# Performance work log

Hardware: AMD Instinct MI355X
Metric: run time of the kernel (lower is better)

The kernel has to match this reference:

```python
import jax, jax.numpy as jnp
from jax import lax
import numpy as np

P = 4        # pool_size
NH = 8       # nhead
EPS = 1e-5


def _maxpool(x):
    return lax.reduce_window(x, -jnp.inf, lax.max, (1, 1, P, P), (1, 1, P, P), 'VALID')


def _ln_c(x, g, b):
    # LayerNorm over channel dim of NCHW (torch applies it on NHWC last dim)
    m = x.mean(1, keepdims=True)
    v = x.var(1, keepdims=True)
    return g[None, :, None, None] * (x - m) / jnp.sqrt(v + EPS) + b[None, :, None, None]


def _dwbn(x, w, g, b, rm, rv):
    # depthwise 3x3 conv (groups=C, no bias) + BatchNorm2d (inference, running stats)
    C = x.shape[1]
    y = lax.conv_general_dilated(x, w, (1, 1), ((1, 1), (1, 1)),
                                 dimension_numbers=('NCHW', 'OIHW', 'NCHW'),
                                 feature_group_count=C)
    sc = g / jnp.sqrt(rv + EPS)
    return sc[None, :, None, None] * (y - rm[None, :, None, None]) + b[None, :, None, None]


def _heads(x):
    # n (nhead d) h w -> n (h w) nhead d
    B, C, H, W = x.shape
    return x.reshape(B, NH, C // NH, H * W).transpose(0, 3, 1, 2)


def _fuse(x, m, merge_w, mlp_w1, mlp_w2, ln2_g, ln2_b):
    # merge linear -> reshape to pooled map -> bilinear upsample x4 -> concat -> MLP -> LN -> residual
    B, C, H, W = x.shape
    m = jnp.einsum('nlh d -> nlhd', m) if False else m  # no-op, keep m as [B,L,NH,dim]
    m = m.reshape(B, -1, C) @ merge_w.T                  # [B, L, C]
    m = m.reshape(B, H // P, W // P, C).transpose(0, 3, 1, 2)
    m = jax.image.resize(m, (B, C, H, W), method='bilinear')  # align_corners=False convention
    z = jnp.concatenate([x, m], axis=1).transpose(0, 2, 3, 1)  # NHWC, 2C
    z = jax.nn.relu(z @ mlp_w1.T) @ mlp_w2.T                   # [B,H,W,C]
    mu = z.mean(-1, keepdims=True)
    var = z.var(-1, keepdims=True)
    z = ln2_g * (z - mu) / jnp.sqrt(var + EPS) + ln2_b
    return x + z.transpose(0, 3, 1, 2)


def setup_inputs() -> dict:
    key = jax.random.key(0)
    ks = jax.random.split(key, 20)
    B, C, H, W = 4, 256, 128, 128
    s = 0.05
    return {
        'x1': jax.random.normal(ks[0], (B, C, H, W), jnp.float32),
        'x2': jax.random.normal(ks[1], (B, C, H, W), jnp.float32),
        'qk_w': jax.random.normal(ks[2], (C, 1, 3, 3), jnp.float32) * s,
        'qk_g': 1.0 + 0.1 * jax.random.normal(ks[3], (C,), jnp.float32),
        'qk_b': 0.1 * jax.random.normal(ks[4], (C,), jnp.float32),
        'qk_m': 0.1 * jax.random.normal(ks[5], (C,), jnp.float32),
        'qk_v': jax.random.uniform(ks[6], (C,), jnp.float32, 0.5, 1.5),
        'v_w': jax.random.normal(ks[7], (C, 1, 3, 3), jnp.float32) * s,
        'v_g': 1.0 + 0.1 * jax.random.normal(ks[8], (C,), jnp.float32),
        'v_b': 0.1 * jax.random.normal(ks[9], (C,), jnp.float32),
        'v_m': 0.1 * jax.random.normal(ks[10], (C,), jnp.float32),
        'v_v': jax.random.uniform(ks[11], (C,), jnp.float32, 0.5, 1.5),
        'ln1_g': 1.0 + 0.1 * jax.random.normal(ks[12], (C,), jnp.float32),
        'ln1_b': 0.1 * jax.random.normal(ks[13], (C,), jnp.float32),
        'ln2_g': 1.0 + 0.1 * jax.random.normal(ks[14], (C,), jnp.float32),
        'ln2_b': 0.1 * jax.random.normal(ks[15], (C,), jnp.float32),
        'merge_w': jax.random.normal(ks[16], (C, C), jnp.float32) * s,
        'mlp_w1': jax.random.normal(ks[17], (2 * C, 2 * C), jnp.float32) * s,
        'mlp_w2': jax.random.normal(ks[18], (C, 2 * C), jnp.float32) * s,
    }


def reference(x1, x2, qk_w, qk_g, qk_b, qk_m, qk_v, v_w, v_g, v_b, v_m, v_v,
              ln1_g, ln1_b, ln2_g, ln2_b, merge_w, mlp_w1, mlp_w2):
    # pooled + normalized features (norm1 shared across q/k/v branches)
    p1 = _ln_c(_maxpool(x1), ln1_g, ln1_b)
    p2 = _ln_c(_maxpool(x2), ln1_g, ln1_b)
    query = _heads(_dwbn(p1, qk_w, qk_g, qk_b, qk_m, qk_v))  # [B,L,NH,d]
    key = _heads(_dwbn(p2, qk_w, qk_g, qk_b, qk_m, qk_v))    # [B,S,NH,d]
    v1h = _heads(_dwbn(p1, v_w, v_g, v_b, v_m, v_v))
    v2h = _heads(_dwbn(p2, v_w, v_g, v_b, v_m, v_v))
    QK = jnp.einsum('nlhd,nshd->nlsh', query, key).astype(jnp.float32)
    t = 1.0 / np.sqrt(query.shape[-1]).astype(np.float32)
    S1 = jax.nn.softmax(t * QK, axis=2)   # softmax over s (keys)
    S2 = jax.nn.softmax(t * QK, axis=3)   # softmax over head dim (as in source)
    m1 = jnp.einsum('nlsh,nshd->nlhd', S1, v2h)
    m2 = jnp.einsum('nlsh,nlhd->nshd', S2, v1h)
    out1 = _fuse(x1, m1, merge_w, mlp_w1, mlp_w2, ln2_g, ln2_b)
    out2 = _fuse(x2, m2, merge_w, mlp_w1, mlp_w2, ln2_g, ln2_b)
    return (out1, out2)
```

## Files before the change

### kernel.cpp

```cpp
#include <hip/hip_runtime.h>
#include <hip/hip_bf16.h>

#define NB 4
#define NC 256
#define NH_ 8
#define LPOOL 1024
constexpr float EPSV = 1e-5f;

typedef unsigned short ushort_t;
typedef __attribute__((ext_vector_type(8))) short bf16x8;
typedef __attribute__((ext_vector_type(4))) float f32x4;

#define OFF_P   0u
#define OFF_V2T 1048576u
#define OFF_Q   2097152u
#define OFF_K   3145728u
#define OFF_V1  4194304u
#define OFF_V2  5242880u
#define OFF_M1  6291456u
#define OFF_M2  7340032u
#define OFF_MG  8388608u
#define OFF_A   9437184u
#define OFF_W1B 26214400u
#define OFF_W2B 26345472u
#define OFF_WCB 26411008u

__device__ __forceinline__ float bf16_to_f(unsigned short u) {
    union { unsigned int ui; float f; } t; t.ui = ((unsigned int)u) << 16; return t.f;
}
__device__ __forceinline__ unsigned short f_to_bf16(float f) {
    union { float f; unsigned int u; } t; t.f = f;
    unsigned int u = t.u;
    u += 0x7fffu + ((u >> 16) & 1u);
    return (unsigned short)(u >> 16);
}

__global__ __launch_bounds__(256) void pool_kernel(const float* __restrict__ x1,
                                                   const float* __restrict__ x2,
                                                   float* __restrict__ pooled) {
    int idx = blockIdx.x * 256 + threadIdx.x;
    int j = idx & 31, i = (idx >> 5) & 31, c = (idx >> 10) & 255, n = (idx >> 18) & 3, br = idx >> 20;
    const float* xp = br ? x2 : x1;
    const float* base = xp + (((size_t)(n * 256 + c) * 128 + i * 4) * 128 + j * 4);
    float m = -3.4e38f;
#pragma unroll
    for (int r = 0; r < 4; ++r) {
        float4 v = *(const float4*)(base + r * 128);
        m = fmaxf(m, fmaxf(fmaxf(v.x, v.y), fmaxf(v.z, v.w)));
    }
    pooled[(size_t)br * 1048576 + (size_t)(n * 256 + c) * 1024 + i * 32 + j] = m;
}

__global__ __launch_bounds__(256) void lnc_kernel(float* __restrict__ p,
                                                  const float* __restrict__ g,
                                                  const float* __restrict__ b) {
    int bid = blockIdx.x;
    int l = bid & 1023, n = (bid >> 10) & 3, br = bid >> 12;
    int c = threadIdx.x;
    size_t idx = (size_t)br * 1048576 + (size_t)(n * 256 + c) * 1024 + l;
    float v = p[idx];
    __shared__ float red[256];
    red[c] = v; __syncthreads();
    for (int off = 128; off > 0; off >>= 1) { if (c < off) red[c] += red[c + off]; __syncthreads(); }
    float mean = red[0] / 256.f;
    __syncthreads();
    float d = v - mean;
    red[c] = d * d; __syncthreads();
    for (int off = 128; off > 0; off >>= 1) { if (c < off) red[c] += red[c + off]; __syncthreads(); }
    float var = red[0] / 256.f;
    float rstd = rsqrtf(var + EPSV);
    p[idx] = (v - mean) * rstd * g[c] + b[c];
}

__global__ __launch_bounds__(256) void dwbn_kernel(const float* __restrict__ p,
    const float* __restrict__ qkw, const float* __restrict__ qkg, const float* __restrict__ qkb,
    const float* __restrict__ qkm, const float* __restrict__ qkv,
    const float* __restrict__ vw, const float* __restrict__ vg, const float* __restrict__ vb,
    const float* __restrict__ vm, const float* __restrict__ vv,
    float* __restrict__ qkvbuf) {
    int which = blockIdx.y;
    int flat = blockIdx.x * 256 + threadIdx.x;
    int l = flat & 1023, c = (flat >> 10) & 255, n = flat >> 18;
    int br = which & 1;
    const float* w  = (which < 2) ? qkw : vw;
    const float* g  = (which < 2) ? qkg : vg;
    const float* bb = (which < 2) ? qkb : vb;
    const float* rm = (which < 2) ? qkm : vm;
    const float* rv = (which < 2) ? qkv : vv;
    int i = l >> 5, j = l & 31;
    const float* pin = p + (size_t)br * 1048576 + (size_t)(n * 256 + c) * 1024;
    float acc = 0.f;
#pragma unroll
    for (int ky = -1; ky <= 1; ++ky) {
        int yy = i + ky;
        if ((unsigned)yy < 32u) {
#pragma unroll
            for (int kx = -1; kx <= 1; ++kx) {
                int xx = j + kx;
                if ((unsigned)xx < 32u)
                    acc += pin[yy * 32 + xx] * w[c * 9 + (ky + 1) * 3 + (kx + 1)];
            }
        }
    }
    float sc = g[c] * rsqrtf(rv[c] + EPSV);
    qkvbuf[(size_t)which * 1048576 + (size_t)(n * 1024 + l) * 256 + c] = sc * (acc - rm[c]) + bb[c];
}

__global__ __launch_bounds__(256) void cvt_kernel(const float* __restrict__ in,
                                                  ushort_t* __restrict__ out, int n) {
    int i = blockIdx.x * 256 + threadIdx.x;
    if (i < n) out[i] = f_to_bf16(in[i]);
}

__global__ __launch_bounds__(256) void wc_kernel(const float* __restrict__ w1,
                                                 const float* __restrict__ mw,
                                                 ushort_t* __restrict__ wcb) {
    int r = blockIdx.x, t = threadIdx.x;
    __shared__ float wrow[256];
    wrow[t] = w1[(size_t)r * 512 + 256 + t];
    __syncthreads();
    float acc = 0.f;
    for (int c = 0; c < 256; ++c) acc += wrow[c] * mw[(size_t)c * 256 + t];
    wcb[(size_t)r * 256 + t] = f_to_bf16(acc);
}

__global__ __launch_bounds__(256) void v2t_kernel(const float* __restrict__ v,
                                                  ushort_t* __restrict__ vt) {
    int bid = blockIdx.x;
    int sb = bid & 31, cb = (bid >> 5) & 7, n = bid >> 8;
    int tid = threadIdx.x;
    __shared__ float t[32][33];
    int ci = tid & 31, sg = tid >> 5;
#pragma unroll
    for (int p = 0; p < 4; ++p) {
        int s = sb * 32 + p * 8 + sg;
        t[p * 8 + sg][ci] = v[(size_t)(n * 1024 + s) * 256 + cb * 32 + ci];
    }
    __syncthreads();
    int si = tid & 31, cg = tid >> 5;
#pragma unroll
    for (int p = 0; p < 4; ++p) {
        int c = cb * 32 + p * 8 + cg;
        vt[(size_t)(n * 256 + c) * 1024 + sb * 32 + si] = f_to_bf16(t[si][p * 8 + cg]);
    }
}

__global__ __launch_bounds__(256) void qk_mfma(const ushort_t* __restrict__ qb,
                                               const ushort_t* __restrict__ kb,
                                               ushort_t* __restrict__ scores) {
    int lt = blockIdx.x, st = blockIdx.y;
    int nh = blockIdx.z; int n = nh >> 3, h = nh & 7;
    int l0 = lt * 128, s0 = st * 128;
    __shared__ ushort_t Qs[128 * 32];
    __shared__ ushort_t Ks[128 * 32];
    int tid = threadIdx.x, lane = tid & 63, wv = tid >> 6;
    int wm = wv >> 1, wn = wv & 1;
    int ml = lane & 15, quad = lane >> 4;
#pragma unroll
    for (int c = 0; c < 2; ++c) {
        int g = c * 256 + tid;
        int row = g >> 2, seg = g & 3;
        const ushort_t* ga = qb + (size_t)(n * 1024 + l0 + row) * 256 + h * 32 + seg * 8;
        __builtin_amdgcn_global_load_lds((const __attribute__((address_space(1))) void*)ga,
                                         (__attribute__((address_space(3))) void*)&Qs[row * 32 + seg * 8], 16, 0, 0);
        const ushort_t* gk = kb + (size_t)(n * 1024 + s0 + row) * 256 + h * 32 + seg * 8;
        __builtin_amdgcn_global_load_lds((const __attribute__((address_space(1))) void*)gk,
                                         (__attribute__((address_space(3))) void*)&Ks[row * 32 + seg * 8], 16, 0, 0);
    }
    __syncthreads();
    f32x4 acc[4][4];
#pragma unroll
    for (int i = 0; i < 4; ++i)
#pragma unroll
        for (int j = 0; j < 4; ++j) acc[i][j] = (f32x4)(0.f);
    bf16x8 af[4], bfr[4];
#pragma unroll
    for (int mt = 0; mt < 4; ++mt)
        af[mt] = *(const bf16x8*)&Qs[(wm * 64 + mt * 16 + ml) * 32 + quad * 8];
#pragma unroll
    for (int nt = 0; nt < 4; ++nt)
        bfr[nt] = *(const bf16x8*)&Ks[(wn * 64 + nt * 16 + ml) * 32 + quad * 8];
#pragma unroll
    for (int mt = 0; mt < 4; ++mt)
#pragma unroll
        for (int nt = 0; nt < 4; ++nt)
            acc[mt][nt] = __builtin_amdgcn_mfma_f32_16x16x32_bf16(af[mt], bfr[nt], acc[mt][nt], 0, 0, 0);
    const float tsc = 0.17677669529663687f;
    ushort_t* sb = scores + (size_t)nh * 1024 * 1024;
#pragma unroll
    for (int mt = 0; mt < 4; ++mt)
#pragma unroll
        for (int nt = 0; nt < 4; ++nt) {
            int col = s0 + wn * 64 + nt * 16 + ml;
#pragma unroll
            for (int r = 0; r < 4; ++r) {
                int row = l0 + wm * 64 + mt * 16 + quad * 4 + r;
                unsigned short b = f_to_bf16(tsc * acc[mt][nt][r]);
                int partner = __shfl_xor((int)b, 1);
                if (!(ml & 1)) {
                    unsigned int pk = (unsigned int)b | ((unsigned int)partner << 16);
                    *(unsigned int*)&sb[(size_t)row * 1024 + col] = pk;
                }
            }
        }
}

__global__ __launch_bounds__(256) void m1_kernel(const ushort_t* __restrict__ scores,
                                                 const ushort_t* __restrict__ v2t,
                                                 ushort_t* __restrict__ m1out) {
    int lt = blockIdx.x, h = blockIdx.y, n = blockIdx.z;
    int tid = threadIdx.x, lane = tid & 63, wv = tid >> 6;
    int ml = lane & 15, quad = lane >> 4;
    int l0 = lt * 64 + wv * 16;
    const ushort_t* arow = scores + (size_t)((n * 8 + h) * 1024 + l0 + ml) * 1024 + quad * 8;
    const ushort_t* vb = v2t + (size_t)(n * 256 + h * 32) * 1024;
    const ushort_t* vrow0 = vb + (size_t)ml * 1024 + quad * 8;
    const ushort_t* vrow1 = vb + (size_t)(ml + 16) * 1024 + quad * 8;
    f32x4 acc0 = (f32x4)(0.f), acc1 = (f32x4)(0.f);
    float rsum = 0.f;
#pragma unroll 4
    for (int s0 = 0; s0 < 1024; s0 += 32) {
        bf16x8 sv = *(const bf16x8*)(arow + s0);
        float e0 = __expf(bf16_to_f((ushort_t)sv[0]));
        float e1 = __expf(bf16_to_f((ushort_t)sv[1]));
        float e2 = __expf(bf16_to_f((ushort_t)sv[2]));
        float e3 = __expf(bf16_to_f((ushort_t)sv[3]));
        float e4 = __expf(bf16_to_f((ushort_t)sv[4]));
        float e5 = __expf(bf16_to_f((ushort_t)sv[5]));
        float e6 = __expf(bf16_to_f((ushort_t)sv[6]));
        float e7 = __expf(bf16_to_f((ushort_t)sv[7]));
        rsum += ((e0 + e1) + (e2 + e3)) + ((e4 + e5) + (e6 + e7));
        bf16x8 af;
        af[0] = (short)f_to_bf16(e0); af[1] = (short)f_to_bf16(e1);
        af[2] = (short)f_to_bf16(e2); af[3] = (short)f_to_bf16(e3);
        af[4] = (short)f_to_bf16(e4); af[5] = (short)f_to_bf16(e5);
        af[6] = (short)f_to_bf16(e6); af[7] = (short)f_to_bf16(e7);
        bf16x8 b0 = *(const bf16x8*)(vrow0 + s0);
        bf16x8 b1 = *(const bf16x8*)(vrow1 + s0);
        acc0 = __builtin_amdgcn_mfma_f32_16x16x32_bf16(af, b0, acc0, 0, 0, 0);
        acc1 = __builtin_amdgcn_mfma_f32_16x16x32_bf16(af, b1, acc1, 0, 0, 0);
    }
    rsum += __shfl_xor(rsum, 16);
    rsum += __shfl_xor(rsum, 32);
#pragma unroll
    for (int r = 0; r < 4; ++r) {
        int row = quad * 4 + r;
        float inv = 1.f / __shfl(rsum, row);
        size_t ob = (size_t)(n * 1024 + l0 + row) * 256 + h * 32;
        m1out[ob + ml] = f_to_bf16(acc0[r] * inv);
        m1out[ob + 16 + ml] = f_to_bf16(acc1[r] * inv);
    }
}

__global__ __launch_bounds__(256) void m2_kernel(const ushort_t* __restrict__ scores,
                                                 const float* __restrict__ v1,
                                                 float* __restrict__ m2out) {
    int st = blockIdx.x;
    int lc = blockIdx.y;
    int n  = blockIdx.z;
    int s0 = st * 32, tid = threadIdx.x;
    __shared__ float wls[8][8][32];
    float acc[32];
#pragma unroll
    for (int i = 0; i < 32; ++i) acc[i] = 0.f;
    int lA = tid >> 5, siA = tid & 31;
    int hB = tid >> 5;
    const ushort_t* sbase = scores + (size_t)n * 8 * 1024 * 1024;
    int lend = lc * 128 + 128;
    for (int lb = lc * 128; lb < lend; lb += 8) {
        int l = lb + lA;
        float e[8];
        float mx = -3.4e38f;
#pragma unroll
        for (int h = 0; h < 8; ++h) {
            e[h] = bf16_to_f(sbase[((size_t)h * 1024 + l) * 1024 + s0 + siA]);
            mx = fmaxf(mx, e[h]);
        }
        float sum = 0.f;
#pragma unroll
        for (int h = 0; h < 8; ++h) { e[h] = expf(e[h] - mx); sum += e[h]; }
        float inv = 1.f / sum;
#pragma unroll
        for (int h = 0; h < 8; ++h) wls[lA][h][siA] = e[h] * inv;
        __syncthreads();
#pragma unroll
        for (int ls = 0; ls < 8; ++ls) {
            float v1v = v1[(size_t)(n * 1024 + lb + ls) * 256 + tid];
#pragma unroll
            for (int s4 = 0; s4 < 8; ++s4) {
                float4 w4 = *(const float4*)&wls[ls][hB][s4 * 4];
                acc[s4 * 4]     += w4.x * v1v;
                acc[s4 * 4 + 1] += w4.y * v1v;
                acc[s4 * 4 + 2] += w4.z * v1v;
                acc[s4 * 4 + 3] += w4.w * v1v;
            }
        }
        __syncthreads();
    }
#pragma unroll
    for (int ss = 0; ss < 32; ++ss)
        atomicAdd(&m2out[(size_t)(n * 1024 + s0 + ss) * 256 + tid], acc[ss]);
}

__global__ __launch_bounds__(256) void mfma_gemm(const ushort_t* __restrict__ A,
                                                 const ushort_t* __restrict__ B,
                                                 float* __restrict__ Of,
                                                 ushort_t* __restrict__ Oh,
                                                 int N, int relu, int K) {
    int m0 = blockIdx.x * 128, n0 = blockIdx.y * 128;
    int tid = threadIdx.x;
    __shared__ ushort_t Al[128 * 32];
    __shared__ ushort_t Bl[128 * 32];
    int lane = tid & 63;
    int wv = tid >> 6;
    int wm = wv >> 1, wn = wv & 1;
    int ml = lane & 15, quad = lane >> 4;
    f32x4 acc[4][4];
#pragma unroll
    for (int i = 0; i < 4; ++i)
#pragma unroll
        for (int j = 0; j < 4; ++j) acc[i][j] = (f32x4)(0.f);

    for (int k0 = 0; k0 < K; k0 += 32) {
#pragma unroll
        for (int c = 0; c < 2; ++c) {
            int g = c * 256 + tid;
            int row = g >> 2, seg = g & 3;
            const ushort_t* ga = A + (size_t)(m0 + row) * K + k0 + seg * 8;
            __builtin_amdgcn_global_load_lds((const __attribute__((address_space(1))) void*)ga,
                                             (__attribute__((address_space(3))) void*)&Al[g * 8], 16, 0, 0);
            const ushort_t* gb = B + (size_t)(n0 + row) * K + k0 + seg * 8;
            __builtin_amdgcn_global_load_lds((const __attribute__((address_space(1))) void*)gb,
                                             (__attribute__((address_space(3))) void*)&Bl[g * 8], 16, 0, 0);
        }
        __syncthreads();
        bf16x8 af[4], bfr[4];
#pragma unroll
        for (int mt = 0; mt < 4; ++mt)
            af[mt] = *(const bf16x8*)&Al[(wm * 64 + mt * 16 + ml) * 32 + quad * 8];
#pragma unroll
        for (int nt = 0; nt < 4; ++nt)
            bfr[nt] = *(const bf16x8*)&Bl[(wn * 64 + nt * 16 + ml) * 32 + quad * 8];
#pragma unroll
        for (int mt = 0; mt < 4; ++mt)
#pragma unroll
            for (int nt = 0; nt < 4; ++nt)
                acc[mt][nt] = __builtin_amdgcn_mfma_f32_16x16x32_bf16(af[mt], bfr[nt], acc[mt][nt], 0, 0, 0);
        __syncthreads();
    }
#pragma unroll
    for (int mt = 0; mt < 4; ++mt) {
#pragma unroll
        for (int nt = 0; nt < 4; ++nt) {
            int col = n0 + wn * 64 + nt * 16 + ml;
#pragma unroll
            for (int r = 0; r < 4; ++r) {
                int row = m0 + wm * 64 + mt * 16 + quad * 4 + r;
                float v = acc[mt][nt][r];
                if (relu) v = fmaxf(v, 0.f);
                if (Oh) Oh[(size_t)row * N + col] = f_to_bf16(v);
                else    Of[(size_t)row * N + col] = v;
            }
        }
    }
}

__global__ __launch_bounds__(256) void gemm1_fused(const float* __restrict__ x,
                                                   const ushort_t* __restrict__ W1,
                                                   const ushort_t* __restrict__ mm1,
                                                   ushort_t* __restrict__ hid) {
    __shared__ char smem[49152];
    ushort_t* Abf = (ushort_t*)smem;
    ushort_t* Bl  = (ushort_t*)(smem + 32768);
    float* t32    = (float*)(smem + 32768);
    int m0 = blockIdx.x * 64;
    int n = m0 >> 14, y = (m0 >> 7) & 127, x0 = m0 & 127;
    int n0 = blockIdx.y * 256;
    int tid = threadIdx.x, lane = tid & 63;
    int wv = tid >> 6, ml = lane & 15, quad = lane >> 4;

    const float* xrow = x + ((size_t)(n * 256) * 128 + y) * 128 + x0;
    for (int cb = 0; cb < 256; cb += 32) {
        __syncthreads();
        {
            int l16 = tid & 15, cl = tid >> 4;
#pragma unroll
            for (int pp = 0; pp < 2; ++pp) {
                int c = cb + pp * 16 + cl;
                float4 v = *(const float4*)(xrow + (size_t)c * 16384 + l16 * 4);
                *(float4*)&t32[(pp * 16 + cl) * 68 + l16 * 4] = v;
            }
        }
        __syncthreads();
        {
            int clw = tid & 31, pg = tid >> 5;
#pragma unroll
            for (int k = 0; k < 8; ++k) {
                int pix = pg * 8 + k;
                float v = t32[clw * 68 + pix];
                unsigned byte = ((unsigned)(pix * 256 + cb + clw) * 2u) ^ ((unsigned)(pix & 7) << 4);
                *(ushort_t*)(smem + byte) = f_to_bf16(v);
            }
        }
    }
    __syncthreads();

    f32x4 acc[4][4];
#pragma unroll
    for (int i = 0; i < 4; ++i)
#pragma unroll
        for (int j = 0; j < 4; ++j) acc[i][j] = (f32x4)(0.f);
    for (int k0 = 0; k0 < 256; k0 += 32) {
#pragma unroll
        for (int c = 0; c < 4; ++c) {
            int g = c * 256 + tid;
            int row = g >> 2, seg = g & 3;
            const ushort_t* gb = W1 + (size_t)(n0 + row) * 512 + k0 + seg * 8;
            __builtin_amdgcn_global_load_lds((const __attribute__((address_space(1))) void*)gb,
                                             (__attribute__((address_space(3))) void*)&Bl[g * 8], 16, 0, 0);
        }
        __syncthreads();
        bf16x8 af[4], bfr[4];
#pragma unroll
        for (int mt = 0; mt < 4; ++mt) {
            int pix = mt * 16 + ml;
            unsigned byte = ((unsigned)(pix * 256 + k0 + quad * 8) * 2u) ^ ((unsigned)(pix & 7) << 4);
            af[mt] = *(const bf16x8*)(smem + byte);
        }
#pragma unroll
        for (int nt = 0; nt < 4; ++nt)
            bfr[nt] = *(const bf16x8*)&Bl[(wv * 64 + nt * 16 + ml) * 32 + quad * 8];
#pragma unroll
        for (int mt = 0; mt < 4; ++mt)
#pragma unroll
            for (int nt = 0; nt < 4; ++nt)
                acc[mt][nt] = __builtin_amdgcn_mfma_f32_16x16x32_bf16(af[mt], bfr[nt], acc[mt][nt], 0, 0, 0);
        __syncthreads();
    }

    float iy = y * 0.25f - 0.375f;
    int y0i = (int)floorf(iy);
    float fy = iy - (float)y0i;
    int y0c = max(y0i, 0), y1c = min(y0i + 1, 31);
    const ushort_t* mb0 = mm1 + (size_t)(n * 1024 + y0c * 32) * 512;
    const ushort_t* mb1 = mm1 + (size_t)(n * 1024 + y1c * 32) * 512;
#pragma unroll
    for (int mt = 0; mt < 4; ++mt)
#pragma unroll
        for (int r = 0; r < 4; ++r) {
            int p = mt * 16 + quad * 4 + r;
            int xx = x0 + p;
            float ix = xx * 0.25f - 0.375f;
            int x0i = (int)floorf(ix);
            float fx = ix - (float)x0i;
            int xc0 = max(x0i, 0), xc1 = min(x0i + 1, 31);
#pragma unroll
            for (int nt = 0; nt < 4; ++nt) {
                int col = n0 + wv * 64 + nt * 16 + ml;
                float v00 = bf16_to_f(mb0[(size_t)xc0 * 512 + col]);
                float v01 = bf16_to_f(mb0[(size_t)xc1 * 512 + col]);
                float v10 = bf16_to_f(mb1[(size_t)xc0 * 512 + col]);
                float v11 = bf16_to_f(mb1[(size_t)xc1 * 512 + col]);
                float up = (1.f - fy) * ((1.f - fx) * v00 + fx * v01)
                         + fy * ((1.f - fx) * v10 + fx * v11);
                float v = fmaxf(acc[mt][nt][r] + up, 0.f);
                hid[(size_t)(m0 + p) * 512 + col] = f_to_bf16(v);
            }
        }
}

__global__ __launch_bounds__(256) void gemm2_ln(const ushort_t* __restrict__ hid,
                                                const ushort_t* __restrict__ W2,
                                                const float* __restrict__ xin,
                                                const float* __restrict__ g2,
                                                const float* __restrict__ b2,
                                                float* __restrict__ outp) {
    __shared__ char smem[35584];
    ushort_t* Al = (ushort_t*)smem;
    ushort_t* Bl = (ushort_t*)(smem + 4096);
    int m0 = blockIdx.x * 64;
    int tid = threadIdx.x, lane = tid & 63, wv = tid >> 6;
    int ml = lane & 15, quad = lane >> 4;
    f32x4 acc[4][4];
#pragma unroll
    for (int i = 0; i < 4; ++i)
#pragma unroll
        for (int j = 0; j < 4; ++j) acc[i][j] = (f32x4)(0.f);

    for (int k0 = 0; k0 < 512; k0 += 32) {
        {
            int row = tid >> 2, seg = tid & 3;
            const ushort_t* ga = hid + (size_t)(m0 + row) * 512 + k0 + seg * 8;
            __builtin_amdgcn_global_load_lds((const __attribute__((address_space(1))) void*)ga,
                                             (__attribute__((address_space(3))) void*)&Al[tid * 8], 16, 0, 0);
        }
#pragma unroll
        for (int c = 0; c < 4; ++c) {
            int g = c * 256 + tid;
            int row = g >> 2, seg = g & 3;
            const ushort_t* gb = W2 + (size_t)row * 512 + k0 + seg * 8;
            __builtin_amdgcn_global_load_lds((const __attribute__((address_space(1))) void*)gb,
                                             (__attribute__((address_space(3))) void*)&Bl[g * 8], 16, 0, 0);
        }
        __syncthreads();
        bf16x8 af[4], bfr[4];
#pragma unroll
        for (int mt = 0; mt < 4; ++mt)
            af[mt] = *(const bf16x8*)&Al[(mt * 16 + ml) * 32 + quad * 8];
#pragma unroll
        for (int nt = 0; nt < 4; ++nt)
            bfr[nt] = *(const bf16x8*)&Bl[(wv * 64 + nt * 16 + ml) * 32 + quad * 8];
#pragma unroll
        for (int mt = 0; mt < 4; ++mt)
#pragma unroll
            for (int nt = 0; nt < 4; ++nt)
                acc[mt][nt] = __builtin_amdgcn_mfma_f32_16x16x32_bf16(af[mt], bfr[nt], acc[mt][nt], 0, 0, 0);
        __syncthreads();
    }
    float* redS = (float*)smem;
    float* redQ = (float*)(smem + 1024);
    float* muA  = (float*)(smem + 2048);
    float* rsA  = (float*)(smem + 2304);
    float* olds = (float*)(smem + 2560);
#pragma unroll
    for (int mt = 0; mt < 4; ++mt)
#pragma unroll
        for (int r = 0; r < 4; ++r) {
            float s = 0.f, q = 0.f;
#pragma unroll
            for (int nt = 0; nt < 4; ++nt) { float v = acc[mt][nt][r]; s += v; q += v * v; }
            s += __shfl_xor(s, 1); s += __shfl_xor(s, 2); s += __shfl_xor(s, 4); s += __shfl_xor(s, 8);
            q += __shfl_xor(q, 1); q += __shfl_xor(q, 2); q += __shfl_xor(q, 4); q += __shfl_xor(q, 8);
            if (ml == 0) {
                int row = mt * 16 + quad * 4 + r;
                redS[row * 4 + wv] = s; redQ[row * 4 + wv] = q;
            }
        }
    __syncthreads();
    if (tid < 64) {
        float S = redS[tid * 4] + redS[tid * 4 + 1] + redS[tid * 4 + 2] + redS[tid * 4 + 3];
        float Q = redQ[tid * 4] + redQ[tid * 4 + 1] + redQ[tid * 4 + 2] + redQ[tid * 4 + 3];
        float mu = S * (1.f / 256.f);
        float var = Q * (1.f / 256.f) - mu * mu;
        muA[tid] = mu; rsA[tid] = rsqrtf(var + EPSV);
    }
    __syncthreads();
    int n = m0 >> 14, y = (m0 >> 7) & 127, x0 = m0 & 127;
    int cg = tid >> 5, xi = tid & 31;
#pragma unroll
    for (int half = 0; half < 2; ++half) {
        if ((wv >> 1) == half) {
#pragma unroll
            for (int mt = 0; mt < 4; ++mt)
#pragma unroll
                for (int r = 0; r < 4; ++r) {
                    int row = mt * 16 + quad * 4 + r;
                    float mu = muA[row], rs = rsA[row];
#pragma unroll
                    for (int nt = 0; nt < 4; ++nt) {
                        int col = wv * 64 + nt * 16 + ml;
                        int lc = col - half * 128;
                        olds[row * 129 + lc] = (acc[mt][nt][r] - mu) * rs * g2[col] + b2[col];
                    }
                }
        }
        __syncthreads();
        for (int cc = 0; cc < 16; ++cc) {
            int lc = cc * 8 + cg;
            int c = half * 128 + lc;
            size_t gbase = ((size_t)(n * 256 + c) * 128 + y) * 128 + x0;
#pragma unroll
            for (int xc = 0; xc < 2; ++xc) {
                int p = xc * 32 + xi;
                outp[gbase + p] = xin[gbase + p] + olds[p * 129 + lc];
            }
        }
        __syncthreads();
    }
}

extern "C" void kernel_launch(void* const* d_in, const int* in_sizes, int n_in,
                              void* d_out, int out_size, void* d_ws, size_t ws_size,
                              hipStream_t stream) {
    (void)in_sizes; (void)n_in; (void)out_size; (void)ws_size;
    const float* x1     = (const float*)d_in[0];
    const float* x2     = (const float*)d_in[1];
    const float* qk_w   = (const float*)d_in[2];
    const float* qk_g   = (const float*)d_in[3];
    const float* qk_b   = (const float*)d_in[4];
    const float* qk_m   = (const float*)d_in[5];
    const float* qk_v   = (const float*)d_in[6];
    const float* v_w    = (const float*)d_in[7];
    const float* v_g    = (const float*)d_in[8];
    const float* v_b    = (const float*)d_in[9];
    const float* v_m    = (const float*)d_in[10];
    const float* v_v    = (const float*)d_in[11];
    const float* ln1_g  = (const float*)d_in[12];
    const float* ln1_b  = (const float*)d_in[13];
    const float* ln2_g  = (const float*)d_in[14];
    const float* ln2_b  = (const float*)d_in[15];
    const float* merge_w = (const float*)d_in[16];
    const float* mlp_w1 = (const float*)d_in[17];
    const float* mlp_w2 = (const float*)d_in[18];

    float* ws      = (float*)d_ws;
    float* pooled  = ws + OFF_P;
    float* qkvbuf  = ws + OFF_Q;
    float* v1buf   = ws + OFF_V1;
    float* v2buf   = ws + OFF_V2;
    float* m2buf   = ws + OFF_M2;
    ushort_t* m1b16 = (ushort_t*)(ws + OFF_M1);
    ushort_t* mb16  = (ushort_t*)(ws + OFF_V1);
    ushort_t* mm1b  = (ushort_t*)(ws + OFF_MG);
    ushort_t* scores16 = (ushort_t*)(ws + OFF_A);
    ushort_t* qkb16 = (ushort_t*)(ws + OFF_P);
    ushort_t* v2tb = (ushort_t*)(ws + OFF_V2T);
    ushort_t* hid  = (ushort_t*)(ws + OFF_A);
    ushort_t* w1b  = (ushort_t*)(ws + OFF_W1B);
    ushort_t* w2b  = (ushort_t*)(ws + OFF_W2B);
    ushort_t* wcb  = (ushort_t*)(ws + OFF_WCB);
    float* outp    = (float*)d_out;

    hipMemsetAsync(m2buf, 0, 1048576 * sizeof(float), stream);

    wc_kernel<<<512, 256, 0, stream>>>(mlp_w1, merge_w, wcb);
    pool_kernel<<<8192, 256, 0, stream>>>(x1, x2, pooled);
    lnc_kernel<<<8192, 256, 0, stream>>>(pooled, ln1_g, ln1_b);
    dwbn_kernel<<<dim3(4096, 4), 256, 0, stream>>>(pooled,
        qk_w, qk_g, qk_b, qk_m, qk_v, v_w, v_g, v_b, v_m, v_v, qkvbuf);
    cvt_kernel<<<8192, 256, 0, stream>>>(qkvbuf, qkb16, 2097152);
    v2t_kernel<<<1024, 256, 0, stream>>>(v2buf, v2tb);
    qk_mfma<<<dim3(8, 8, 32), 256, 0, stream>>>(qkb16, qkb16 + 1048576, scores16);
    m1_kernel<<<dim3(16, 8, 4), 256, 0, stream>>>(scores16, v2tb, m1b16);
    m2_kernel<<<dim3(32, 8, 4), 256, 0, stream>>>(scores16, v1buf, m2buf);

    cvt_kernel<<<1024, 256, 0, stream>>>(mlp_w1, w1b, 262144);
    cvt_kernel<<<512, 256, 0, stream>>>(mlp_w2, w2b, 131072);

    for (int br = 0; br < 2; ++br) {
        const float* xin = br ? x2 : x1;
        const ushort_t* mmb;
        if (br == 0) {
            mmb = m1b16;
        } else {
            cvt_kernel<<<4096, 256, 0, stream>>>(m2buf, mb16, 1048576);
            mmb = mb16;
        }
        mfma_gemm<<<dim3(32, 4), 256, 0, stream>>>(mmb, wcb, nullptr, mm1b, 512, 0, 256);
        gemm1_fused<<<dim3(1024, 2), 256, 0, stream>>>(xin, w1b, mm1b, hid);
        gemm2_ln<<<1024, 256, 0, stream>>>(hid, w2b, xin, ln2_g, ln2_b,
                                           outp + (size_t)br * 16777216);
    }
}
```

Before: 685.5 us.

## Fuse bf16 convert and V transpose into dwbn; widen gemm1 to full N

The depthwise conv+BN kernel now writes Q/K directly as bf16, V1 as fp32 and V2 transposed as bf16. This removes the separate cvt and v2t kernels and their fp32 round trips. gemm1_fused now covers all 512 output columns in one 512-thread block, so the x tile is loaded and converted once instead of twice. In exchange, the transposed V2 store from dwbn is strided (uncoalesced), and the larger LDS footprint and block size may lower occupancy.

```diff
diff --git a/kernel.cpp b/kernel.cpp
--- a/kernel.cpp
+++ b/kernel.cpp
@@ -12,7 +12,6 @@
 typedef __attribute__((ext_vector_type(4))) float f32x4;
 
 #define OFF_P   0u
-#define OFF_V2T 1048576u
 #define OFF_Q   2097152u
 #define OFF_K   3145728u
 #define OFF_V1  4194304u
@@ -77,7 +76,7 @@
     const float* __restrict__ qkm, const float* __restrict__ qkv,
     const float* __restrict__ vw, const float* __restrict__ vg, const float* __restrict__ vb,
     const float* __restrict__ vm, const float* __restrict__ vv,
-    float* __restrict__ qkvbuf) {
+    ushort_t* __restrict__ qk16, float* __restrict__ v1f, ushort_t* __restrict__ v2t16) {
     int which = blockIdx.y;
     int flat = blockIdx.x * 256 + threadIdx.x;
     int l = flat & 1023, c = (flat >> 10) & 255, n = flat >> 18;
@@ -103,7 +102,13 @@
         }
     }
     float sc = g[c] * rsqrtf(rv[c] + EPSV);
-    qkvbuf[(size_t)which * 1048576 + (size_t)(n * 1024 + l) * 256 + c] = sc * (acc - rm[c]) + bb[c];
+    float r = sc * (acc - rm[c]) + bb[c];
+    if (which < 2)
+        qk16[(size_t)which * 1048576 + (size_t)(n * 1024 + l) * 256 + c] = f_to_bf16(r);
+    else if (which == 2)
+        v1f[(size_t)(n * 1024 + l) * 256 + c] = r;
+    else
+        v2t16[(size_t)(n * 256 + c) * 1024 + l] = f_to_bf16(r);
 }
 
 __global__ __launch_bounds__(256) void cvt_kernel(const float* __restrict__ in,
@@ -122,27 +127,6 @@
     float acc = 0.f;
     for (int c = 0; c < 256; ++c) acc += wrow[c] * mw[(size_t)c * 256 + t];
     wcb[(size_t)r * 256 + t] = f_to_bf16(acc);
-}
-
-__global__ __launch_bounds__(256) void v2t_kernel(const float* __restrict__ v,
-                                                  ushort_t* __restrict__ vt) {
-    int bid = blockIdx.x;
-    int sb = bid & 31, cb = (bid >> 5) & 7, n = bid >> 8;
-    int tid = threadIdx.x;
-    __shared__ float t[32][33];
-    int ci = tid & 31, sg = tid >> 5;
-#pragma unroll
-    for (int p = 0; p < 4; ++p) {
-        int s = sb * 32 + p * 8 + sg;
-        t[p * 8 + sg][ci] = v[(size_t)(n * 1024 + s) * 256 + cb * 32 + ci];
-    }
-    __syncthreads();
-    int si = tid & 31, cg = tid >> 5;
-#pragma unroll
-    for (int p = 0; p < 4; ++p) {
-        int c = cb * 32 + p * 8 + cg;
-        vt[(size_t)(n * 256 + c) * 1024 + sb * 32 + si] = f_to_bf16(t[si][p * 8 + cg]);
-    }
 }
 
 __global__ __launch_bounds__(256) void qk_mfma(const ushort_t* __restrict__ qb,
@@ -365,17 +349,15 @@
     }
 }
 
-__global__ __launch_bounds__(256) void gemm1_fused(const float* __restrict__ x,
+__global__ __launch_bounds__(512) void gemm1_fused(const float* __restrict__ x,
                                                    const ushort_t* __restrict__ W1,
                                                    const ushort_t* __restrict__ mm1,
                                                    ushort_t* __restrict__ hid) {
-    __shared__ char smem[49152];
-    ushort_t* Abf = (ushort_t*)smem;
+    __shared__ char smem[65536];
     ushort_t* Bl  = (ushort_t*)(smem + 32768);
     float* t32    = (float*)(smem + 32768);
     int m0 = blockIdx.x * 64;
     int n = m0 >> 14, y = (m0 >> 7) & 127, x0 = m0 & 127;
-    int n0 = blockIdx.y * 256;
     int tid = threadIdx.x, lane = tid & 63;
     int wv = tid >> 6, ml = lane & 15, quad = lane >> 4;
 
@@ -384,19 +366,15 @@
         __syncthreads();
         {
             int l16 = tid & 15, cl = tid >> 4;
-#pragma unroll
-            for (int pp = 0; pp < 2; ++pp) {
-                int c = cb + pp * 16 + cl;
-                float4 v = *(const float4*)(xrow + (size_t)c * 16384 + l16 * 4);
-                *(float4*)&t32[(pp * 16 + cl) * 68 + l16 * 4] = v;
-            }
+            float4 v = *(const float4*)(xrow + (size_t)(cb + cl) * 16384 + l16 * 4);
+            *(float4*)&t32[cl * 68 + l16 * 4] = v;
         }
         __syncthreads();
         {
             int clw = tid & 31, pg = tid >> 5;
 #pragma unroll
-            for (int k = 0; k < 8; ++k) {
-                int pix = pg * 8 + k;
+            for (int k = 0; k < 4; ++k) {
+                int pix = pg * 4 + k;
                 float v = t32[clw * 68 + pix];
                 unsigned byte = ((unsigned)(pix * 256 + cb + clw) * 2u) ^ ((unsigned)(pix & 7) << 4);
                 *(ushort_t*)(smem + byte) = f_to_bf16(v);
@@ -413,9 +391,9 @@
     for (int k0 = 0; k0 < 256; k0 += 32) {
 #pragma unroll
         for (int c = 0; c < 4; ++c) {
-            int g = c * 256 + tid;
+            int g = c * 512 + tid;
             int row = g >> 2, seg = g & 3;
-            const ushort_t* gb = W1 + (size_t)(n0 + row) * 512 + k0 + seg * 8;
+            const ushort_t* gb = W1 + (size_t)row * 512 + k0 + seg * 8;
             __builtin_amdgcn_global_load_lds((const __attribute__((address_space(1))) void*)gb,
                                              (__attribute__((address_space(3))) void*)&Bl[g * 8], 16, 0, 0);
         }
@@ -456,7 +434,7 @@
             int xc0 = max(x0i, 0), xc1 = min(x0i + 1, 31);
 #pragma unroll
             for (int nt = 0; nt < 4; ++nt) {
-                int col = n0 + wv * 64 + nt * 16 + ml;
+                int col = wv * 64 + nt * 16 + ml;
                 float v00 = bf16_to_f(mb0[(size_t)xc0 * 512 + col]);
                 float v01 = bf16_to_f(mb0[(size_t)xc1 * 512 + col]);
                 float v10 = bf16_to_f(mb1[(size_t)xc0 * 512 + col]);
@@ -605,16 +583,14 @@
 
     float* ws      = (float*)d_ws;
     float* pooled  = ws + OFF_P;
-    float* qkvbuf  = ws + OFF_Q;
     float* v1buf   = ws + OFF_V1;
-    float* v2buf   = ws + OFF_V2;
     float* m2buf   = ws + OFF_M2;
+    ushort_t* qkb16 = (ushort_t*)(ws + OFF_Q);
+    ushort_t* v2tb = (ushort_t*)(ws + OFF_K);
     ushort_t* m1b16 = (ushort_t*)(ws + OFF_M1);
     ushort_t* mb16  = (ushort_t*)(ws + OFF_V1);
     ushort_t* mm1b  = (ushort_t*)(ws + OFF_MG);
     ushort_t* scores16 = (ushort_t*)(ws + OFF_A);
-    ushort_t* qkb16 = (ushort_t*)(ws + OFF_P);
-    ushort_t* v2tb = (ushort_t*)(ws + OFF_V2T);
     ushort_t* hid  = (ushort_t*)(ws + OFF_A);
     ushort_t* w1b  = (ushort_t*)(ws + OFF_W1B);
     ushort_t* w2b  = (ushort_t*)(ws + OFF_W2B);
@@ -627,9 +603,8 @@
     pool_kernel<<<8192, 256, 0, stream>>>(x1, x2, pooled);
     lnc_kernel<<<8192, 256, 0, stream>>>(pooled, ln1_g, ln1_b);
     dwbn_kernel<<<dim3(4096, 4), 256, 0, stream>>>(pooled,
-        qk_w, qk_g, qk_b, qk_m, qk_v, v_w, v_g, v_b, v_m, v_v, qkvbuf);
-    cvt_kernel<<<8192, 256, 0, stream>>>(qkvbuf, qkb16, 2097152);
-    v2t_kernel<<<1024, 256, 0, stream>>>(v2buf, v2tb);
+        qk_w, qk_g, qk_b, qk_m, qk_v, v_w, v_g, v_b, v_m, v_v,
+        qkb16, v1buf, v2tb);
     qk_mfma<<<dim3(8, 8, 32), 256, 0, stream>>>(qkb16, qkb16 + 1048576, scores16);
     m1_kernel<<<dim3(16, 8, 4), 256, 0, stream>>>(scores16, v2tb, m1b16);
     m2_kernel<<<dim3(32, 8, 4), 256, 0, stream>>>(scores16, v1buf, m2buf);
@@ -647,7 +622,7 @@
             mmb = mb16;
         }
         mfma_gemm<<<dim3(32, 4), 256, 0, stream>>>(mmb, wcb, nullptr, mm1b, 512, 0, 256);
-        gemm1_fused<<<dim3(1024, 2), 256, 0, stream>>>(xin, w1b, mm1b, hid);
+        gemm1_fused<<<1024, 512, 0, stream>>>(xin, w1b, mm1b, hid);
         gemm2_ln<<<1024, 256, 0, stream>>>(hid, w2b, xin, ln2_g, ln2_b,
                                            outp + (size_t)br * 16777216);
     }
```

New measurement: 661.7 us. 1.04x faster.
